# Optimization experiments

Measured on AMD Instinct MI355X. Metric: run time of the kernel, lower is better.

## Reference

```python
import jax, jax.numpy as jnp
import numpy as np

D_MODEL = 512
EPS = 1e-5


def setup_inputs() -> dict:
    key = jax.random.key(0)
    k1, k2, k3 = jax.random.split(key, 3)
    B, N, D = 8, 2048, D_MODEL
    output = jax.random.normal(k1, (B, N, D), dtype=jnp.float32)
    # multiplicative 0/1 float mask over the [B, N, N] score matrix
    slf_attn_mask = jax.random.randint(k2, (B, N, N), 0, 2).astype(jnp.float32)
    # nn.Linear(d_model, d_model): weight [out, in], xavier-uniform; bias zeros-ish
    limit = float(np.sqrt(6.0 / (D + D)))
    W = jax.random.uniform(k3, (D, D), dtype=jnp.float32, minval=-limit, maxval=limit)
    b = jnp.zeros((D,), dtype=jnp.float32)
    return {"output": output, "slf_attn_mask": slf_attn_mask, "W": W, "b": b}


def reference(output, slf_attn_mask, W, b):
    temperature = jnp.asarray(D_MODEL, output.dtype) ** 0.5
    # scores: [B, N, N] = (q / temp) @ k^T, then multiplicative mask
    attn = jnp.einsum("bnd,bmd->bnm", output / temperature, output) * slf_attn_mask
    # F.normalize(p=2, dim=-1, eps=1e-5): x / max(||x||_2, eps)
    norm = jnp.sqrt(jnp.sum(attn * attn, axis=-1, keepdims=True))
    attn = attn / jnp.maximum(norm, EPS)
    # values: elu(Linear(output)), Linear uses W @ x + b with W [out, in]
    v = jax.nn.elu(jnp.einsum("bnd,ed->bne", output, W) + b)
    return jnp.einsum("bnm,bme->bne", attn, v)
```

## Files before the change

### kernel.cpp

```cpp
#include <hip/hip_runtime.h>
#include <hip/hip_bf16.h>

#define NSEQ 2048
#define DM 512
#define BATCH 8
#define GTOT (BATCH * NSEQ)
#define INV_T 0.044194173824159216f
#define EPSN 1e-5f

typedef __bf16 bf16_t;
typedef bf16_t bf16x8 __attribute__((ext_vector_type(8)));
typedef float f32x4 __attribute__((ext_vector_type(4)));
typedef unsigned short u16;
typedef unsigned int u32;

__device__ __forceinline__ u16 f2bf(float f) {
    u32 u = __builtin_bit_cast(u32, f);
    u32 r = (u + 0x7FFFu + ((u >> 16) & 1u)) >> 16;
    return (u16)r;
}

__global__ __launch_bounds__(256) void k_convert(
    const float* __restrict__ X, const float* __restrict__ W,
    u16* __restrict__ Kbf, u16* __restrict__ Wbf) {
    const long NK = (long)GTOT * DM / 4;
    const long NW = (long)DM * DM / 4;
    long i = (long)blockIdx.x * 256 + threadIdx.x;
    if (i < NK) {
        float4 f = ((const float4*)X)[i];
        ushort4 o;
        o.x = f2bf(f.x); o.y = f2bf(f.y); o.z = f2bf(f.z); o.w = f2bf(f.w);
        ((ushort4*)Kbf)[i] = o;
    } else if (i < NK + NW) {
        long j = i - NK;
        float4 f = ((const float4*)W)[j];
        ushort4 o;
        o.x = f2bf(f.x); o.y = f2bf(f.y); o.z = f2bf(f.z); o.w = f2bf(f.w);
        ((ushort4*)Wbf)[j] = o;
    }
}

__global__ __launch_bounds__(256, 2) void k_vgemm(
    const u16* __restrict__ Wbf, const u16* __restrict__ Kbf,
    const float* __restrict__ bias, u16* __restrict__ vT) {
    __shared__ __attribute__((aligned(16))) u16 Ks[32 * 520];
    const int tid = threadIdx.x;
    const int wave = tid >> 6, lane = tid & 63, quad = lane >> 4, l15 = lane & 15;
    const int etile = blockIdx.x & 7;
    const int mblk = blockIdx.x >> 3;
    const int ebase = etile * 64 + wave * 16;

    bf16x8 wf[16];
    {
        const u16* wp = Wbf + (long)(ebase + l15) * DM + quad * 8;
#pragma unroll
        for (int ks = 0; ks < 16; ++ks) wf[ks] = *(const bf16x8*)(wp + ks * 32);
    }
    float bvals[4];
#pragma unroll
    for (int r = 0; r < 4; ++r) bvals[r] = bias[ebase + quad * 4 + r];

    bf16x8 kreg[8];
    {
        const int g0 = mblk * 256;
#pragma unroll
        for (int j = 0; j < 8; ++j) {
            int c = tid + 256 * j;
            int row = c >> 6, col = c & 63;
            kreg[j] = *(const bf16x8*)(Kbf + (long)(g0 + row) * DM + col * 8);
        }
    }
    for (int mt = 0; mt < 8; ++mt) {
        const int g0 = mblk * 256 + mt * 32;
        __syncthreads();
#pragma unroll
        for (int j = 0; j < 8; ++j) {
            int c = tid + 256 * j;
            int row = c >> 6, col = c & 63;
            *(bf16x8*)(&Ks[row * 520 + col * 8]) = kreg[j];
        }
        __syncthreads();
        {
            int mtn = (mt + 1 < 8) ? mt + 1 : 0;
            const int gn = mblk * 256 + mtn * 32;
#pragma unroll
            for (int j = 0; j < 8; ++j) {
                int c = tid + 256 * j;
                int row = c >> 6, col = c & 63;
                kreg[j] = *(const bf16x8*)(Kbf + (long)(gn + row) * DM + col * 8);
            }
        }
        f32x4 acc[2] = {{0.f, 0.f, 0.f, 0.f}, {0.f, 0.f, 0.f, 0.f}};
#pragma unroll
        for (int ks = 0; ks < 16; ++ks) {
#pragma unroll
            for (int nt = 0; nt < 2; ++nt) {
                bf16x8 kf = *(const bf16x8*)(&Ks[(nt * 16 + l15) * 520 + ks * 32 + quad * 8]);
                acc[nt] = __builtin_amdgcn_mfma_f32_16x16x32_bf16(wf[ks], kf, acc[nt], 0, 0, 0);
            }
        }
#pragma unroll
        for (int nt = 0; nt < 2; ++nt) {
#pragma unroll
            for (int r = 0; r < 4; ++r) {
                int e = ebase + quad * 4 + r;
                int g = g0 + nt * 16 + l15;
                float x = acc[nt][r] + bvals[r];
                float v = x > 0.f ? x : (__expf(x) - 1.f);
                vT[(long)e * GTOT + g] = f2bf(v);
            }
        }
    }
}

__global__ __launch_bounds__(256, 1) void k_flash(
    const u16* __restrict__ Kbf, const u16* __restrict__ vT,
    const float* __restrict__ mask, float* __restrict__ Out) {
    __shared__ __attribute__((aligned(16))) u16 KV[512 * 40];
    __shared__ __attribute__((aligned(16))) u16 Sb[4][16 * 40];
    const int tid = threadIdx.x;
    const int wave = tid >> 6, lane = tid & 63, quad = lane >> 4, l15 = lane & 15;
    const int b = blockIdx.x >> 5;
    const int rblk = blockIdx.x & 31;
    const int r0 = rblk * 64 + wave * 16;

    bf16x8 qf[16];
    {
        const u16* qp = Kbf + (long)(b * NSEQ + r0 + l15) * DM + quad * 8;
#pragma unroll
        for (int ks = 0; ks < 16; ++ks) qf[ks] = *(const bf16x8*)(qp + ks * 32);
    }
    f32x4 oacc[32];
#pragma unroll
    for (int i = 0; i < 32; ++i) oacc[i] = (f32x4){0.f, 0.f, 0.f, 0.f};
    float ss[4] = {0.f, 0.f, 0.f, 0.f};

    const float* mrow = mask + (long)(b * NSEQ + r0 + quad * 4) * NSEQ;
    const u16* kbase = Kbf + (long)b * NSEQ * DM;
    const u16* vbase = vT + (long)b * NSEQ;

    bf16x8 kreg[8];
    float mv[8];
#pragma unroll
    for (int j = 0; j < 8; ++j) {
        int c = tid + 256 * j;
        int row = c >> 6, col = c & 63;
        kreg[j] = *(const bf16x8*)(kbase + (long)row * DM + col * 8);
    }
#pragma unroll
    for (int q = 0; q < 8; ++q) {
        int nt = q >> 2, r = q & 3;
        mv[q] = mrow[(long)r * NSEQ + nt * 16 + l15];
    }

    for (int mt = 0; mt < 64; ++mt) {
        const int m0 = mt * 32;
        __syncthreads();
#pragma unroll
        for (int j = 0; j < 8; ++j) {
            int c = tid + 256 * j;
            int row = c >> 6, col = c & 63;
            *(bf16x8*)(&KV[row * 520 + col * 8]) = kreg[j];
        }
        __syncthreads();
        bf16x8 vreg[8];
#pragma unroll
        for (int dh = 0; dh < 2; ++dh) {
            int d = tid + dh * 256;
            const u16* vp = vbase + (long)d * GTOT + m0;
#pragma unroll
            for (int j = 0; j < 4; ++j) vreg[dh * 4 + j] = *(const bf16x8*)(vp + j * 8);
        }
        f32x4 sacc[2] = {{0.f, 0.f, 0.f, 0.f}, {0.f, 0.f, 0.f, 0.f}};
#pragma unroll
        for (int ks = 0; ks < 16; ++ks) {
#pragma unroll
            for (int nt = 0; nt < 2; ++nt) {
                bf16x8 kf = *(const bf16x8*)(&KV[(nt * 16 + l15) * 520 + ks * 32 + quad * 8]);
                sacc[nt] = __builtin_amdgcn_mfma_f32_16x16x32_bf16(qf[ks], kf, sacc[nt], 0, 0, 0);
            }
        }
#pragma unroll
        for (int nt = 0; nt < 2; ++nt) {
#pragma unroll
            for (int r = 0; r < 4; ++r) {
                float s = sacc[nt][r] * mv[nt * 4 + r] * INV_T;
                ss[r] += s * s;
                Sb[wave][(quad * 4 + r) * 40 + nt * 16 + l15] = f2bf(s);
            }
        }
        __syncthreads();
#pragma unroll
        for (int dh = 0; dh < 2; ++dh) {
            int d = tid + dh * 256;
#pragma unroll
            for (int j = 0; j < 4; ++j) *(bf16x8*)(&KV[d * 40 + j * 8]) = vreg[dh * 4 + j];
        }
        {
            int mtn = (mt + 1 < 64) ? mt + 1 : 0;
            const int mn = mtn * 32;
#pragma unroll
            for (int j = 0; j < 8; ++j) {
                int c = tid + 256 * j;
                int row = c >> 6, col = c & 63;
                kreg[j] = *(const bf16x8*)(kbase + (long)(mn + row) * DM + col * 8);
            }
#pragma unroll
            for (int q = 0; q < 8; ++q) {
                int nt = q >> 2, r = q & 3;
                mv[q] = mrow[(long)r * NSEQ + mn + nt * 16 + l15];
            }
        }
        __syncthreads();
        bf16x8 af = *(const bf16x8*)(&Sb[wave][l15 * 40 + quad * 8]);
#pragma unroll
        for (int nt = 0; nt < 32; ++nt) {
            bf16x8 vf = *(const bf16x8*)(&KV[(nt * 16 + l15) * 40 + quad * 8]);
            oacc[nt] = __builtin_amdgcn_mfma_f32_16x16x32_bf16(af, vf, oacc[nt], 0, 0, 0);
        }
    }
#pragma unroll
    for (int r = 0; r < 4; ++r) {
        float v = ss[r];
        v += __shfl_xor(v, 1, 16);
        v += __shfl_xor(v, 2, 16);
        v += __shfl_xor(v, 4, 16);
        v += __shfl_xor(v, 8, 16);
        ss[r] = 1.f / fmaxf(sqrtf(v), EPSN);
    }
    float* op = Out + (long)(b * NSEQ + r0 + quad * 4) * DM + l15;
#pragma unroll
    for (int nt = 0; nt < 32; ++nt) {
#pragma unroll
        for (int r = 0; r < 4; ++r) op[(long)r * DM + nt * 16] = oacc[nt][r] * ss[r];
    }
}

extern "C" void kernel_launch(void* const* d_in, const int* in_sizes, int n_in,
                              void* d_out, int out_size, void* d_ws, size_t ws_size,
                              hipStream_t stream) {
    const float* X = (const float*)d_in[0];
    const float* mask = (const float*)d_in[1];
    const float* W = (const float*)d_in[2];
    const float* bias = (const float*)d_in[3];
    float* out = (float*)d_out;

    char* ws = (char*)d_ws;
    u16* Kbf = (u16*)ws;
    u16* Wbf = (u16*)(ws + 16777216);
    u16* vT = (u16*)(ws + 16777216 + 524288);

    k_convert<<<8448, 256, 0, stream>>>(X, W, Kbf, Wbf);
    k_vgemm<<<512, 256, 0, stream>>>(Wbf, Kbf, bias, vT);
    k_flash<<<256, 256, 0, stream>>>(Kbf, vT, mask, out);
}
```

Before: 372.5 us.

## Restructure flash kernel to 8 waves, 64-key tiles and 32x32 MFMA for PV

Result: faster. 360.3 us (-3.3%).

```diff
diff --git a/kernel.cpp b/kernel.cpp
--- a/kernel.cpp
+++ b/kernel.cpp
@@ -11,6 +11,7 @@
 typedef __bf16 bf16_t;
 typedef bf16_t bf16x8 __attribute__((ext_vector_type(8)));
 typedef float f32x4 __attribute__((ext_vector_type(4)));
+typedef float f32x16 __attribute__((ext_vector_type(16)));
 typedef unsigned short u16;
 typedef unsigned int u32;
 
@@ -113,39 +114,53 @@
     }
 }
 
-__global__ __launch_bounds__(256, 1) void k_flash(
+__global__ __launch_bounds__(512, 2) void k_flash(
     const u16* __restrict__ Kbf, const u16* __restrict__ vT,
     const float* __restrict__ mask, float* __restrict__ Out) {
-    __shared__ __attribute__((aligned(16))) u16 KV[512 * 40];
-    __shared__ __attribute__((aligned(16))) u16 Sb[4][16 * 40];
+    extern __shared__ char smem[];
+    u16* Ks = (u16*)smem;
+    u16* Vs = (u16*)(smem + 66560);
+    u16* Ss = (u16*)(smem + 66560 + 73728);
+    float* ssred = (float*)(smem + 149504);
+
     const int tid = threadIdx.x;
-    const int wave = tid >> 6, lane = tid & 63, quad = lane >> 4, l15 = lane & 15;
+    const int wave = tid >> 6, lane = tid & 63;
+    const int quad = lane >> 4, l15 = lane & 15;
+    const int l31 = lane & 31, lh = lane >> 5;
+    const int rg = wave >> 1, kh = wave & 1;
+    const int rgp = wave >> 2, dq = wave & 3;
     const int b = blockIdx.x >> 5;
     const int rblk = blockIdx.x & 31;
-    const int r0 = rblk * 64 + wave * 16;
+    const int row0 = rblk * 64;
 
     bf16x8 qf[16];
     {
-        const u16* qp = Kbf + (long)(b * NSEQ + r0 + l15) * DM + quad * 8;
+        const u16* qp = Kbf + (long)(b * NSEQ + row0 + rg * 16 + l15) * DM + quad * 8;
 #pragma unroll
         for (int ks = 0; ks < 16; ++ks) qf[ks] = *(const bf16x8*)(qp + ks * 32);
     }
-    f32x4 oacc[32];
-#pragma unroll
-    for (int i = 0; i < 32; ++i) oacc[i] = (f32x4){0.f, 0.f, 0.f, 0.f};
+    f32x16 oacc[4];
+#pragma unroll
+    for (int i = 0; i < 4; ++i)
+#pragma unroll
+        for (int j = 0; j < 16; ++j) oacc[i][j] = 0.f;
     float ss[4] = {0.f, 0.f, 0.f, 0.f};
 
-    const float* mrow = mask + (long)(b * NSEQ + r0 + quad * 4) * NSEQ;
     const u16* kbase = Kbf + (long)b * NSEQ * DM;
     const u16* vbase = vT + (long)b * NSEQ;
-
-    bf16x8 kreg[8];
+    const float* mrow = mask + (long)(b * NSEQ + row0 + rg * 16 + quad * 4) * NSEQ + kh * 32;
+
+    bf16x8 kreg[8], vreg[8];
     float mv[8];
 #pragma unroll
     for (int j = 0; j < 8; ++j) {
-        int c = tid + 256 * j;
-        int row = c >> 6, col = c & 63;
-        kreg[j] = *(const bf16x8*)(kbase + (long)row * DM + col * 8);
+        int c = tid + 512 * j;
+        kreg[j] = *(const bf16x8*)(kbase + (long)(c >> 6) * DM + (c & 63) * 8);
+    }
+#pragma unroll
+    for (int j = 0; j < 8; ++j) {
+        int c = tid + 512 * j;
+        vreg[j] = *(const bf16x8*)(vbase + (long)(c >> 3) * GTOT + (c & 7) * 8);
     }
 #pragma unroll
     for (int q = 0; q < 8; ++q) {
@@ -153,30 +168,25 @@
         mv[q] = mrow[(long)r * NSEQ + nt * 16 + l15];
     }
 
-    for (int mt = 0; mt < 64; ++mt) {
-        const int m0 = mt * 32;
-        __syncthreads();
-#pragma unroll
-        for (int j = 0; j < 8; ++j) {
-            int c = tid + 256 * j;
-            int row = c >> 6, col = c & 63;
-            *(bf16x8*)(&KV[row * 520 + col * 8]) = kreg[j];
-        }
-        __syncthreads();
-        bf16x8 vreg[8];
-#pragma unroll
-        for (int dh = 0; dh < 2; ++dh) {
-            int d = tid + dh * 256;
-            const u16* vp = vbase + (long)d * GTOT + m0;
-#pragma unroll
-            for (int j = 0; j < 4; ++j) vreg[dh * 4 + j] = *(const bf16x8*)(vp + j * 8);
-        }
+    for (int mt = 0; mt < 32; ++mt) {
+        __syncthreads();
+#pragma unroll
+        for (int j = 0; j < 8; ++j) {
+            int c = tid + 512 * j;
+            *(bf16x8*)(&Ks[(c >> 6) * 520 + (c & 63) * 8]) = kreg[j];
+        }
+#pragma unroll
+        for (int j = 0; j < 8; ++j) {
+            int c = tid + 512 * j;
+            *(bf16x8*)(&Vs[(c >> 3) * 72 + (c & 7) * 8]) = vreg[j];
+        }
+        __syncthreads();
         f32x4 sacc[2] = {{0.f, 0.f, 0.f, 0.f}, {0.f, 0.f, 0.f, 0.f}};
 #pragma unroll
         for (int ks = 0; ks < 16; ++ks) {
 #pragma unroll
             for (int nt = 0; nt < 2; ++nt) {
-                bf16x8 kf = *(const bf16x8*)(&KV[(nt * 16 + l15) * 520 + ks * 32 + quad * 8]);
+                bf16x8 kf = *(const bf16x8*)(&Ks[(kh * 32 + nt * 16 + l15) * 520 + ks * 32 + quad * 8]);
                 sacc[nt] = __builtin_amdgcn_mfma_f32_16x16x32_bf16(qf[ks], kf, sacc[nt], 0, 0, 0);
             }
         }
@@ -186,24 +196,22 @@
             for (int r = 0; r < 4; ++r) {
                 float s = sacc[nt][r] * mv[nt * 4 + r] * INV_T;
                 ss[r] += s * s;
-                Sb[wave][(quad * 4 + r) * 40 + nt * 16 + l15] = f2bf(s);
-            }
-        }
-        __syncthreads();
-#pragma unroll
-        for (int dh = 0; dh < 2; ++dh) {
-            int d = tid + dh * 256;
-#pragma unroll
-            for (int j = 0; j < 4; ++j) *(bf16x8*)(&KV[d * 40 + j * 8]) = vreg[dh * 4 + j];
-        }
+                Ss[(rg * 16 + quad * 4 + r) * 72 + kh * 32 + nt * 16 + l15] = f2bf(s);
+            }
+        }
+        __syncthreads();
         {
-            int mtn = (mt + 1 < 64) ? mt + 1 : 0;
-            const int mn = mtn * 32;
+            int mtn = (mt + 1) & 31;
+            const int mn = mtn * 64;
 #pragma unroll
             for (int j = 0; j < 8; ++j) {
-                int c = tid + 256 * j;
-                int row = c >> 6, col = c & 63;
-                kreg[j] = *(const bf16x8*)(kbase + (long)(mn + row) * DM + col * 8);
+                int c = tid + 512 * j;
+                kreg[j] = *(const bf16x8*)(kbase + (long)(mn + (c >> 6)) * DM + (c & 63) * 8);
+            }
+#pragma unroll
+            for (int j = 0; j < 8; ++j) {
+                int c = tid + 512 * j;
+                vreg[j] = *(const bf16x8*)(vbase + (long)(c >> 3) * GTOT + mn + (c & 7) * 8);
             }
 #pragma unroll
             for (int q = 0; q < 8; ++q) {
@@ -211,12 +219,14 @@
                 mv[q] = mrow[(long)r * NSEQ + mn + nt * 16 + l15];
             }
         }
-        __syncthreads();
-        bf16x8 af = *(const bf16x8*)(&Sb[wave][l15 * 40 + quad * 8]);
-#pragma unroll
-        for (int nt = 0; nt < 32; ++nt) {
-            bf16x8 vf = *(const bf16x8*)(&KV[(nt * 16 + l15) * 40 + quad * 8]);
-            oacc[nt] = __builtin_amdgcn_mfma_f32_16x16x32_bf16(af, vf, oacc[nt], 0, 0, 0);
+#pragma unroll
+        for (int kk = 0; kk < 4; ++kk) {
+            bf16x8 af = *(const bf16x8*)(&Ss[(rgp * 32 + l31) * 72 + kk * 16 + lh * 8]);
+#pragma unroll
+            for (int dt = 0; dt < 4; ++dt) {
+                bf16x8 vf = *(const bf16x8*)(&Vs[(dq * 128 + dt * 32 + l31) * 72 + kk * 16 + lh * 8]);
+                oacc[dt] = __builtin_amdgcn_mfma_f32_32x32x16_bf16(af, vf, oacc[dt], 0, 0, 0);
+            }
         }
     }
 #pragma unroll
@@ -226,13 +236,18 @@
         v += __shfl_xor(v, 2, 16);
         v += __shfl_xor(v, 4, 16);
         v += __shfl_xor(v, 8, 16);
-        ss[r] = 1.f / fmaxf(sqrtf(v), EPSN);
-    }
-    float* op = Out + (long)(b * NSEQ + r0 + quad * 4) * DM + l15;
-#pragma unroll
-    for (int nt = 0; nt < 32; ++nt) {
-#pragma unroll
-        for (int r = 0; r < 4; ++r) op[(long)r * DM + nt * 16] = oacc[nt][r] * ss[r];
+        if (l15 == 0) ssred[wave * 16 + quad * 4 + r] = v;
+    }
+    __syncthreads();
+#pragma unroll
+    for (int reg = 0; reg < 16; ++reg) {
+        int rowoff = (reg & 3) + 8 * (reg >> 2) + 4 * lh;
+        int R = rgp * 32 + rowoff;
+        float tot = ssred[(R >> 4) * 32 + (R & 15)] + ssred[(R >> 4) * 32 + 16 + (R & 15)];
+        float sc = 1.f / fmaxf(sqrtf(tot), EPSN);
+        float* op = Out + (long)(b * NSEQ + row0 + R) * DM + dq * 128 + l31;
+#pragma unroll
+        for (int dt = 0; dt < 4; ++dt) op[dt * 32] = oacc[dt][reg] * sc;
     }
 }
 
@@ -252,5 +267,5 @@
 
     k_convert<<<8448, 256, 0, stream>>>(X, W, Kbf, Wbf);
     k_vgemm<<<512, 256, 0, stream>>>(Wbf, Kbf, bias, vT);
-    k_flash<<<256, 256, 0, stream>>>(Kbf, vT, mask, out);
-}
+    k_flash<<<256, 512, 150016, stream>>>(Kbf, vT, mask, out);
+}
```
